# Kernel tuning notes

Hardware: AMD Instinct MI355X
Metric: run time of the kernel (lower is better)

The kernel has to match this reference:

```python
import jax, jax.numpy as jnp
import numpy as np

IN, E, T = 1024, 512, 4096

def _lstm_dir(xs, Wih, Whh, b):
    # xs: [T, E]; Wih: [4E, E]; Whh: [4E, E]; b: [4E] (b_ih + b_hh)
    H = Whh.shape[1]
    def step(carry, xt):
        h, c = carry
        g = xt @ Wih.T + h @ Whh.T + b  # [4E], torch gate order: i, f, g, o
        i, f, gg, o = jnp.split(g, 4)
        i = jax.nn.sigmoid(i); f = jax.nn.sigmoid(f)
        gg = jnp.tanh(gg); o = jax.nn.sigmoid(o)
        c = f * c + i * gg
        h = o * jnp.tanh(c)
        return (h, c), h
    init = (jnp.zeros((H,), xs.dtype), jnp.zeros((H,), xs.dtype))
    _, hs = jax.lax.scan(step, init, xs)
    return hs  # [T, H]

def setup_inputs() -> dict:
    key = jax.random.key(0)
    ks = jax.random.split(key, 12)
    inp = {
        "x": jax.random.normal(ks[0], (1, T, IN), jnp.float32),
        "A": jax.random.normal(ks[1], (IN, E), jnp.float32) * 0.02,
        "B": jax.random.normal(ks[2], (IN, E), jnp.float32) * 0.02,
        "U": jax.random.normal(ks[3], (IN, E), jnp.float32) * 0.02,
        "w_ih_f": jax.random.normal(ks[4], (4 * E, E), jnp.float32) * 0.05,
        "w_hh_f": jax.random.normal(ks[5], (4 * E, E), jnp.float32) * 0.05,
        "b_ih_f": jax.random.normal(ks[6], (4 * E,), jnp.float32) * 0.05,
        "b_hh_f": jnp.zeros((4 * E,), jnp.float32),
        "w_ih_b": jax.random.normal(ks[7], (4 * E, E), jnp.float32) * 0.05,
        "w_hh_b": jax.random.normal(ks[8], (4 * E, E), jnp.float32) * 0.05,
        "b_ih_b": jax.random.normal(ks[9], (4 * E,), jnp.float32) * 0.05,
        "b_hh_b": jnp.zeros((4 * E,), jnp.float32),
        "final_w": jax.random.normal(ks[10], (1, 2 * E), jnp.float32) * 0.05,
        "final_b": jnp.zeros((1,), jnp.float32),
    }
    return inp

def reference(x, A, B, U, w_ih_f, w_hh_f, b_ih_f, b_hh_f,
              w_ih_b, w_hh_b, b_ih_b, b_hh_b, final_w, final_b):
    a = jnp.einsum('bti,ie->bte', x, A)  # [1,T,E]
    b = jnp.einsum('bti,ie->bte', x, B)
    u = jnp.einsum('bti,ie->bte', x, U)
    scores = jnp.einsum('bqe,bke->bqk', u, a)      # unscaled attention [1,T,T]
    p = jax.nn.softmax(scores, axis=-1)
    out_vec = jnp.einsum('bqk,bke->bqe', p, b)     # [1,T,E]
    u_mod = (u * out_vec)[0]                       # gate, batch=1 -> [T,E]
    hf = _lstm_dir(u_mod, w_ih_f, w_hh_f, b_ih_f + b_hh_f)
    hb = _lstm_dir(u_mod[::-1], w_ih_b, w_hh_b, b_ih_b + b_hh_b)[::-1]
    otp = jnp.concatenate([hf, hb], axis=-1)[None]  # [1,T,2E]
    score = jnp.einsum('bte,oe->bto', otp, final_w) + final_b  # [1,T,1]
    return score
```

## Files before the change

### kernel.cpp

```cpp
#include <hip/hip_runtime.h>
#include <cstddef>
#include <cstdint>

#define T_   4096
#define IN_  1024
#define E_   512
#define G4_  2048

typedef unsigned short ushort_t;
typedef __attribute__((ext_vector_type(8))) short bf16x8;
typedef __attribute__((ext_vector_type(4))) float f32x4;

__device__ __forceinline__ ushort_t rne_bf16(float x) {
    unsigned int u = __float_as_uint(x);
    return (ushort_t)((u + 0x7FFFu + ((u >> 16) & 1u)) >> 16);
}
__device__ __forceinline__ float bf2f(ushort_t h) {
    return __uint_as_float((unsigned int)h << 16);
}

__device__ __forceinline__ unsigned long long load_l2_u64(const unsigned long long* p) {
    unsigned long long v;
    asm volatile("global_load_dwordx2 %0, %1, off sc0\n\ts_waitcnt vmcnt(0)"
                 : "=v"(v) : "v"(p) : "memory");
    return v;
}

__global__ __launch_bounds__(256) void mfma_gemm(
    const ushort_t* __restrict__ Ah, const ushort_t* __restrict__ Al,
    const ushort_t* __restrict__ Bh, const ushort_t* __restrict__ Bl,
    float* __restrict__ Cf, ushort_t* __restrict__ Ch, ushort_t* __restrict__ Cl,
    int M, int N, int K, int nA,
    const float* __restrict__ bias1, const float* __restrict__ bias2)
{
    __shared__ ushort_t sAh[128 * 40], sAl[128 * 40];
    __shared__ ushort_t sBh[128 * 40], sBl[128 * 40];

    const int tid  = threadIdx.x;
    const int wv   = tid >> 6;
    const int lane = tid & 63;
    const int quad = lane >> 4;
    const int l16  = lane & 15;
    const int bm = blockIdx.y * 128, bn = blockIdx.x * 128;
    const int wrow = (wv & 1) * 64, wcol = (wv >> 1) * 64;

    f32x4 acc[4][4];
#pragma unroll
    for (int i = 0; i < 4; ++i)
#pragma unroll
        for (int j = 0; j < 4; ++j) acc[i][j] = (f32x4){0.f, 0.f, 0.f, 0.f};

    const int r0 = tid >> 2;
    const int ks = (tid & 3) * 8;

    for (int k0 = 0; k0 < K; k0 += 32) {
        const size_t ga0 = (size_t)(bm + r0) * K + k0 + ks;
        const size_t ga1 = (size_t)(bm + r0 + 64) * K + k0 + ks;
        const size_t gb0 = (size_t)(bn + r0) * K + k0 + ks;
        const size_t gb1 = (size_t)(bn + r0 + 64) * K + k0 + ks;
        uint4 vA0 = *(const uint4*)(Ah + ga0);
        uint4 vA1 = *(const uint4*)(Ah + ga1);
        uint4 vB0h = *(const uint4*)(Bh + gb0);
        uint4 vB1h = *(const uint4*)(Bh + gb1);
        uint4 vB0l = *(const uint4*)(Bl + gb0);
        uint4 vB1l = *(const uint4*)(Bl + gb1);
        uint4 vA0l, vA1l;
        if (nA == 2) { vA0l = *(const uint4*)(Al + ga0); vA1l = *(const uint4*)(Al + ga1); }
        __syncthreads();
        *(uint4*)&sAh[r0 * 40 + ks] = vA0;
        *(uint4*)&sAh[(r0 + 64) * 40 + ks] = vA1;
        *(uint4*)&sBh[r0 * 40 + ks] = vB0h;
        *(uint4*)&sBh[(r0 + 64) * 40 + ks] = vB1h;
        *(uint4*)&sBl[r0 * 40 + ks] = vB0l;
        *(uint4*)&sBl[(r0 + 64) * 40 + ks] = vB1l;
        if (nA == 2) {
            *(uint4*)&sAl[r0 * 40 + ks] = vA0l;
            *(uint4*)&sAl[(r0 + 64) * 40 + ks] = vA1l;
        }
        __syncthreads();

        bf16x8 afh[4], afl[4], bfh[4], bfl[4];
#pragma unroll
        for (int f = 0; f < 4; ++f) {
            const int ar = (wrow + f * 16 + l16) * 40 + quad * 8;
            const int br = (wcol + f * 16 + l16) * 40 + quad * 8;
            afh[f] = *(const bf16x8*)&sAh[ar];
            bfh[f] = *(const bf16x8*)&sBh[br];
            bfl[f] = *(const bf16x8*)&sBl[br];
            if (nA == 2) afl[f] = *(const bf16x8*)&sAl[ar];
        }
#pragma unroll
        for (int fi = 0; fi < 4; ++fi)
#pragma unroll
            for (int fj = 0; fj < 4; ++fj) {
                acc[fi][fj] = __builtin_amdgcn_mfma_f32_16x16x32_bf16(
                    afh[fi], bfh[fj], acc[fi][fj], 0, 0, 0);
                acc[fi][fj] = __builtin_amdgcn_mfma_f32_16x16x32_bf16(
                    afh[fi], bfl[fj], acc[fi][fj], 0, 0, 0);
                if (nA == 2)
                    acc[fi][fj] = __builtin_amdgcn_mfma_f32_16x16x32_bf16(
                        afl[fi], bfh[fj], acc[fi][fj], 0, 0, 0);
            }
    }

#pragma unroll
    for (int fi = 0; fi < 4; ++fi)
#pragma unroll
        for (int fj = 0; fj < 4; ++fj) {
            const int col = bn + wcol + fj * 16 + l16;
            float bv = 0.f;
            if (bias1) bv += bias1[col];
            if (bias2) bv += bias2[col];
#pragma unroll
            for (int r = 0; r < 4; ++r) {
                const int row = bm + wrow + fi * 16 + quad * 4 + r;
                const float v = acc[fi][fj][r] + bv;
                const size_t o = (size_t)row * N + col;
                if (Cf) Cf[o] = v;
                if (Ch) {
                    const ushort_t h = rne_bf16(v);
                    Ch[o] = h;
                    if (Cl) Cl[o] = rne_bf16(v - bf2f(h));
                }
            }
        }
}

__global__ __launch_bounds__(256) void conv_hl(
    const float* __restrict__ in, ushort_t* __restrict__ oh, ushort_t* __restrict__ ol)
{
    const size_t i = ((size_t)blockIdx.x * 256 + threadIdx.x) * 4;
    float4 v = *(const float4*)(in + i);
    ushort4 h, l;
    h.x = rne_bf16(v.x); l.x = rne_bf16(v.x - bf2f(h.x));
    h.y = rne_bf16(v.y); l.y = rne_bf16(v.y - bf2f(h.y));
    h.z = rne_bf16(v.z); l.z = rne_bf16(v.z - bf2f(h.z));
    h.w = rne_bf16(v.w); l.w = rne_bf16(v.w - bf2f(h.w));
    *(ushort4*)(oh + i) = h;
    *(ushort4*)(ol + i) = l;
}

__global__ __launch_bounds__(256) void conv_hl_T(
    const float* __restrict__ in, ushort_t* __restrict__ oh, ushort_t* __restrict__ ol,
    int R, int C)
{
    __shared__ float t[32][33];
    const int tx = threadIdx.x & 31, ty = threadIdx.x >> 5;
    const int gr = blockIdx.y * 32, gc = blockIdx.x * 32;
#pragma unroll
    for (int i = 0; i < 4; ++i)
        t[ty + 8 * i][tx] = in[(size_t)(gr + ty + 8 * i) * C + gc + tx];
    __syncthreads();
#pragma unroll
    for (int i = 0; i < 4; ++i) {
        const int oc = gc + ty + 8 * i;
        const float v = t[tx][ty + 8 * i];
        const ushort_t h = rne_bf16(v);
        oh[(size_t)oc * R + gr + tx] = h;
        ol[(size_t)oc * R + gr + tx] = rne_bf16(v - bf2f(h));
    }
}

__global__ __launch_bounds__(256) void softmax_kernel(
    const float* __restrict__ S, ushort_t* __restrict__ P)
{
    __shared__ float red[8];
    const float* p = S + (size_t)blockIdx.x * T_;
    ushort_t* pr = P + (size_t)blockIdx.x * T_;
    const int tid = threadIdx.x;
    const int wid = tid >> 6;
    const int lane = tid & 63;
    float4 v[4];
#pragma unroll
    for (int i = 0; i < 4; ++i) v[i] = ((const float4*)p)[tid + 256 * i];
    float m = -3.0e38f;
#pragma unroll
    for (int i = 0; i < 4; ++i)
        m = fmaxf(m, fmaxf(fmaxf(v[i].x, v[i].y), fmaxf(v[i].z, v[i].w)));
#pragma unroll
    for (int o = 32; o; o >>= 1) m = fmaxf(m, __shfl_xor(m, o));
    if (lane == 0) red[wid] = m;
    __syncthreads();
    m = fmaxf(fmaxf(red[0], red[1]), fmaxf(red[2], red[3]));
    float s = 0.f;
#pragma unroll
    for (int i = 0; i < 4; ++i) {
        v[i].x = __expf(v[i].x - m); v[i].y = __expf(v[i].y - m);
        v[i].z = __expf(v[i].z - m); v[i].w = __expf(v[i].w - m);
        s += v[i].x + v[i].y + v[i].z + v[i].w;
    }
#pragma unroll
    for (int o = 32; o; o >>= 1) s += __shfl_xor(s, o);
    if (lane == 0) red[4 + wid] = s;
    __syncthreads();
    s = red[4] + red[5] + red[6] + red[7];
    const float inv = 1.f / s;
#pragma unroll
    for (int i = 0; i < 4; ++i) {
        ushort4 o4;
        o4.x = rne_bf16(v[i].x * inv); o4.y = rne_bf16(v[i].y * inv);
        o4.z = rne_bf16(v[i].z * inv); o4.w = rne_bf16(v[i].w * inv);
        ((ushort4*)pr)[tid + 256 * i] = o4;
    }
}

__global__ __launch_bounds__(256) void umod_kernel(
    const ushort_t* __restrict__ uh, const ushort_t* __restrict__ ul,
    const float* __restrict__ ov,
    ushort_t* __restrict__ mh, ushort_t* __restrict__ ml)
{
    const size_t i = ((size_t)blockIdx.x * 256 + threadIdx.x) * 4;
    ushort4 h4 = *(const ushort4*)(uh + i);
    ushort4 l4 = *(const ushort4*)(ul + i);
    float4 o = *(const float4*)(ov + i);
    float4 m;
    m.x = (bf2f(h4.x) + bf2f(l4.x)) * o.x;
    m.y = (bf2f(h4.y) + bf2f(l4.y)) * o.y;
    m.z = (bf2f(h4.z) + bf2f(l4.z)) * o.z;
    m.w = (bf2f(h4.w) + bf2f(l4.w)) * o.w;
    ushort4 oh, ol;
    oh.x = rne_bf16(m.x); ol.x = rne_bf16(m.x - bf2f(oh.x));
    oh.y = rne_bf16(m.y); ol.y = rne_bf16(m.y - bf2f(oh.y));
    oh.z = rne_bf16(m.z); ol.z = rne_bf16(m.z - bf2f(oh.z));
    oh.w = rne_bf16(m.w); ol.w = rne_bf16(m.w - bf2f(oh.w));
    *(ushort4*)(mh + i) = oh;
    *(ushort4*)(ml + i) = ol;
}

#define NU_ 16
#define PACE_L 8L
#define PACE_A 25L

__global__ __launch_bounds__(256, 1) void lstm_kernel(
    const float* __restrict__ whh_f, const float* __restrict__ whh_b,
    const ushort_t* __restrict__ xg_f, const ushort_t* __restrict__ xg_b,
    float* __restrict__ hf_out, float* __restrict__ hb_out,
    unsigned int* __restrict__ hbuf,
    unsigned int* __restrict__ lbuf)
{
    const int xcd = blockIdx.x & 7;
    if (xcd >= 2) return;
    const int dir = xcd;
    const int w   = blockIdx.x >> 3;

    __shared__ float sh[2][4 * 132];

    const int tid  = threadIdx.x;
    const int lane = tid & 63;
    const int j    = tid >> 4;
    const int g    = (tid >> 2) & 3;
    const int c    = tid & 3;
    const int lu   = lane >> 4;
    const int u0   = w * NU_;

    const float* whh = dir ? whh_b : whh_f;
    const ushort_t* xg = dir ? xg_b : xg_f;
    float* hout = dir ? hb_out : hf_out;
    unsigned int* hb = hbuf + dir * 1024;
    unsigned int* lb = lbuf + dir * 1024;

    float wreg[128];
    {
        const float* wr = whh + (size_t)(g * E_ + u0 + j) * E_ + 128 * c;
#pragma unroll
        for (int i = 0; i < 32; ++i)
            *(float4*)&wreg[4 * i] = *(const float4*)(wr + 4 * i);
    }
    for (int i = tid; i < 2 * 4 * 132; i += 256) ((float*)sh)[i] = 0.f;

    float creg = 0.f;
    const float gsc  = (g == 2) ? 2.f : 1.f;
    const float gmul = (g == 2) ? 2.f : 1.f;
    const float gadd = (g == 2) ? -1.f : 0.f;

    float xv = bf2f(xg[(size_t)(dir ? (T_ - 1) : 0) * G4_ + g * E_ + u0 + j]);
    unsigned int budget = 1u << 23;

    const int e0 = 2 * tid;
    const int p0 = (e0 >> 7) * 132 + (e0 & 127);

    long long tpub = (long long)__builtin_amdgcn_s_memrealtime();
    int use_local = 1, failcnt = 0;

    for (int s = 0; s < T_; ++s) {
        const int t = dir ? (T_ - 1 - s) : s;

        if (s > 0) {
            const long long pt = use_local ? PACE_L : PACE_A;
            while ((long long)__builtin_amdgcn_s_memrealtime() - tpub < pt) {}
            const unsigned int tt = (unsigned int)(s - 1) & 0xFFFFu;
            const unsigned long long* srcL =
                (const unsigned long long*)(lb + ((s - 1) & 1) * 512);
            const unsigned long long* srcA =
                (const unsigned long long*)(hb + ((s - 1) & 1) * 512);
            unsigned long long v;
            if (use_local) {
                bool fell = false;
                int spins = 0;
                for (;;) {
                    v = load_l2_u64(srcL + tid);
                    if (((unsigned int)v >> 16) == tt &&
                        ((unsigned int)(v >> 32) >> 16) == tt) break;
                    if (++spins >= 6) {
                        v = __hip_atomic_load(srcA + tid, __ATOMIC_RELAXED,
                                              __HIP_MEMORY_SCOPE_AGENT);
                        if (((unsigned int)v >> 16) == tt &&
                            ((unsigned int)(v >> 32) >> 16) == tt) { fell = true; break; }
                        if (!--budget) break;
                    }
                }
                if (__ballot(fell)) { if (++failcnt >= 8) use_local = 0; }
                else failcnt = 0;
            } else {
                for (;;) {
                    v = __hip_atomic_load(srcA + tid, __ATOMIC_RELAXED,
                                          __HIP_MEMORY_SCOPE_AGENT);
                    if ((((unsigned int)v >> 16) == tt &&
                         ((unsigned int)(v >> 32) >> 16) == tt) || !--budget) break;
                }
            }
            float2 hv;
            hv.x = __uint_as_float((unsigned int)v << 16);
            hv.y = __uint_as_float((unsigned int)(v >> 32) << 16);
            *(float2*)&sh[s & 1][p0] = hv;
        }
        __syncthreads();

        const float* hc = &sh[s & 1][132 * c];
        float sx = 0.f, sy = 0.f, sz = 0.f, sw = 0.f;
#pragma unroll
        for (int i = 0; i < 32; ++i) {
            const float4 h4 = *(const float4*)&hc[4 * i];
            sx = fmaf(wreg[4 * i + 0], h4.x, sx);
            sy = fmaf(wreg[4 * i + 1], h4.y, sy);
            sz = fmaf(wreg[4 * i + 2], h4.z, sz);
            sw = fmaf(wreg[4 * i + 3], h4.w, sw);
        }
        float sum = (sx + sy) + (sz + sw);
        sum += __shfl_xor(sum, 1);
        sum += __shfl_xor(sum, 2);

        const float xx = (sum + xv) * gsc;
        const float rr = __builtin_amdgcn_rcpf(1.f + __expf(-xx));
        const float val = fmaf(rr, gmul, gadd);

        const int base = 16 * lu + c;
        const float iv = __shfl(val, base);
        const float fv = __shfl(val, base + 4);
        const float gv = __shfl(val, base + 8);
        const float ov = __shfl(val, base + 12);
        creg = fmaf(fv, creg, iv * gv);
        const float th = fmaf(2.f, __builtin_amdgcn_rcpf(1.f + __expf(-2.f * creg)), -1.f);
        const float h = ov * th;

        if ((tid & 15) == 0) {
            const unsigned int ub = __float_as_uint(h);
            const unsigned int b16 = (ub + 0x7FFFu + ((ub >> 16) & 1u)) >> 16;
            const unsigned int pkt = (((unsigned int)s & 0xFFFFu) << 16) | b16;
            __hip_atomic_store(lb + (s & 1) * 512 + u0 + j, pkt,
                               __ATOMIC_RELAXED, __HIP_MEMORY_SCOPE_WORKGROUP);
            __hip_atomic_store(hb + (s & 1) * 512 + u0 + j, pkt,
                               __ATOMIC_RELAXED, __HIP_MEMORY_SCOPE_AGENT);
            hout[(size_t)t * E_ + u0 + j] = h;
        }
        tpub = (long long)__builtin_amdgcn_s_memrealtime();

        if (s + 1 < T_)
            xv = bf2f(xg[(size_t)(dir ? (T_ - 2 - s) : (s + 1)) * G4_ + g * E_ + u0 + j]);
    }
}

__global__ __launch_bounds__(256) void final_kernel(
    const float* __restrict__ hf, const float* __restrict__ hb,
    const float* __restrict__ fw, const float* __restrict__ fb,
    float* __restrict__ out)
{
    const int t = blockIdx.x * 4 + (threadIdx.x >> 6);
    const int lane = threadIdx.x & 63;
    float s = 0.f;
#pragma unroll
    for (int i = 0; i < 8; ++i) {
        const int e = lane + 64 * i;
        s += hf[(size_t)t * E_ + e] * fw[e];
    }
#pragma unroll
    for (int i = 0; i < 8; ++i) {
        const int e = lane + 64 * i;
        s += hb[(size_t)t * E_ + e] * fw[E_ + e];
    }
#pragma unroll
    for (int o = 32; o; o >>= 1) s += __shfl_xor(s, o);
    if (lane == 0) out[t] = s + fb[0];
}

extern "C" void kernel_launch(void* const* d_in, const int* in_sizes, int n_in,
                              void* d_out, int out_size, void* d_ws, size_t ws_size,
                              hipStream_t stream)
{
    const float* x     = (const float*)d_in[0];
    const float* Amat  = (const float*)d_in[1];
    const float* Bmat  = (const float*)d_in[2];
    const float* Umat  = (const float*)d_in[3];
    const float* wih_f = (const float*)d_in[4];
    const float* whh_f = (const float*)d_in[5];
    const float* bih_f = (const float*)d_in[6];
    const float* bhh_f = (const float*)d_in[7];
    const float* wih_b = (const float*)d_in[8];
    const float* whh_b = (const float*)d_in[9];
    const float* bih_b = (const float*)d_in[10];
    const float* bhh_b = (const float*)d_in[11];
    const float* fw    = (const float*)d_in[12];
    const float* fb    = (const float*)d_in[13];
    float* out = (float*)d_out;
    char* wsb = (char*)d_ws;
    const size_t MB = 1048576ull;

    ushort_t* uh  = (ushort_t*)(wsb + 0 * MB);
    ushort_t* ul  = (ushort_t*)(wsb + 4 * MB);
    float*    bfp = (float*)   (wsb + 8 * MB);
    ushort_t* xh  = (ushort_t*)(wsb + 16 * MB);
    ushort_t* xl  = (ushort_t*)(wsb + 24 * MB);
    ushort_t* ATh = (ushort_t*)(wsb + 32 * MB);
    ushort_t* ATl = (ushort_t*)(wsb + 33 * MB);
    ushort_t* BTh = (ushort_t*)(wsb + 34 * MB);
    ushort_t* BTl = (ushort_t*)(wsb + 35 * MB);
    ushort_t* UTh = (ushort_t*)(wsb + 36 * MB);
    ushort_t* UTl = (ushort_t*)(wsb + 37 * MB);
    ushort_t* ah  = (ushort_t*)(wsb + 38 * MB);
    ushort_t* al  = (ushort_t*)(wsb + 42 * MB);
    ushort_t* bTh = (ushort_t*)(wsb + 46 * MB);
    ushort_t* bTl = (ushort_t*)(wsb + 50 * MB);
    float*    S_  = (float*)   (wsb + 56 * MB);
    ushort_t* Ph  = (ushort_t*)(wsb + 8 * MB);
    float*    ov_ = (float*)   (wsb + 56 * MB);
    ushort_t* umh = (ushort_t*)(wsb + 64 * MB);
    ushort_t* uml = (ushort_t*)(wsb + 68 * MB);
    ushort_t* wfh = (ushort_t*)(wsb + 72 * MB);
    ushort_t* wfl = (ushort_t*)(wsb + 74 * MB);
    ushort_t* wbh = (ushort_t*)(wsb + 76 * MB);
    ushort_t* wbl = (ushort_t*)(wsb + 78 * MB);
    ushort_t* xfg = (ushort_t*)(wsb + 80 * MB);
    ushort_t* xbg = (ushort_t*)(wsb + 96 * MB);
    float*    hf_ = (float*)   (wsb + 0 * MB);
    float*    hb_ = (float*)   (wsb + 8 * MB);
    unsigned int* hbuf_ = (unsigned int*)(wsb + 112 * MB);
    unsigned int* lbuf_ = (unsigned int*)(wsb + 113 * MB);

    dim3 blk(256);

    conv_hl<<<dim3(4096), blk, 0, stream>>>(x, xh, xl);
    conv_hl_T<<<dim3(16, 32), blk, 0, stream>>>(Amat, ATh, ATl, 1024, 512);
    conv_hl_T<<<dim3(16, 32), blk, 0, stream>>>(Bmat, BTh, BTl, 1024, 512);
    conv_hl_T<<<dim3(16, 32), blk, 0, stream>>>(Umat, UTh, UTl, 1024, 512);
    mfma_gemm<<<dim3(4, 32), blk, 0, stream>>>(xh, xl, ATh, ATl, nullptr, ah, al,
                                               T_, E_, IN_, 2, nullptr, nullptr);
    mfma_gemm<<<dim3(4, 32), blk, 0, stream>>>(xh, xl, BTh, BTl, bfp, nullptr, nullptr,
                                               T_, E_, IN_, 2, nullptr, nullptr);
    mfma_gemm<<<dim3(4, 32), blk, 0, stream>>>(xh, xl, UTh, UTl, nullptr, uh, ul,
                                               T_, E_, IN_, 2, nullptr, nullptr);
    mfma_gemm<<<dim3(32, 32), blk, 0, stream>>>(uh, ul, ah, al, S_, nullptr, nullptr,
                                                T_, T_, E_, 2, nullptr, nullptr);
    conv_hl_T<<<dim3(16, 128), blk, 0, stream>>>(bfp, bTh, bTl, 4096, 512);
    softmax_kernel<<<dim3(T_), blk, 0, stream>>>(S_, Ph);
    mfma_gemm<<<dim3(4, 32), blk, 0, stream>>>(Ph, nullptr, bTh, bTl, ov_, nullptr, nullptr,
                                               T_, E_, T_, 1, nullptr, nullptr);
    umod_kernel<<<dim3(2048), blk, 0, stream>>>(uh, ul, ov_, umh, uml);
    conv_hl<<<dim3(1024), blk, 0, stream>>>(wih_f, wfh, wfl);
    conv_hl<<<dim3(1024), blk, 0, stream>>>(wih_b, wbh, wbl);
    mfma_gemm<<<dim3(16, 32), blk, 0, stream>>>(umh, uml, wfh, wfl, nullptr, xfg, nullptr,
                                                T_, G4_, E_, 2, bih_f, bhh_f);
    mfma_gemm<<<dim3(16, 32), blk, 0, stream>>>(umh, uml, wbh, wbl, nullptr, xbg, nullptr,
                                                T_, G4_, E_, 2, bih_b, bhh_b);
    lstm_kernel<<<dim3(256), blk, 0, stream>>>(whh_f, whh_b, xfg, xbg, hf_, hb_,
                                               hbuf_, lbuf_);
    final_kernel<<<dim3(1024), blk, 0, stream>>>(hf_, hb_, fw, fb, out);
}
```

Before: 6.739 ms.

## Replace per-step block barrier with per-wave h gathering and startup mode consensus

Each wave now loads the whole 512-element previous hidden state into its own LDS slice and polls tags itself, which removes the per-timestep __syncthreads. A one-time probe at kernel start checks whether workgroup-scope L2 stores are visible to all 32 blocks of a direction. The blocks then agree on a single mode, local L2 or agent scope, and store only to that buffer instead of writing both and falling back dynamically. In exchange each wave issues four times as many polling loads per step, uses more LDS, and relies on the startup probe being a correct test of cross-CU visibility.

```diff
diff --git a/kernel.cpp b/kernel.cpp
--- a/kernel.cpp
+++ b/kernel.cpp
@@ -24,6 +24,21 @@
     asm volatile("global_load_dwordx2 %0, %1, off sc0\n\ts_waitcnt vmcnt(0)"
                  : "=v"(v) : "v"(p) : "memory");
     return v;
+}
+__device__ __forceinline__ unsigned int load_l2_u32(const unsigned int* p) {
+    unsigned int v;
+    asm volatile("global_load_dword %0, %1, off sc0\n\ts_waitcnt vmcnt(0)"
+                 : "=v"(v) : "v"(p) : "memory");
+    return v;
+}
+
+__device__ __forceinline__ bool tags8(unsigned long long a, unsigned long long b,
+                                      unsigned long long c, unsigned long long d,
+                                      unsigned int tt) {
+    return ((unsigned int)a >> 16) == tt && (unsigned int)(a >> 48) == tt &&
+           ((unsigned int)b >> 16) == tt && (unsigned int)(b >> 48) == tt &&
+           ((unsigned int)c >> 16) == tt && (unsigned int)(c >> 48) == tt &&
+           ((unsigned int)d >> 16) == tt && (unsigned int)(d >> 48) == tt;
 }
 
 __global__ __launch_bounds__(256) void mfma_gemm(
@@ -236,16 +251,20 @@
     const ushort_t* __restrict__ xg_f, const ushort_t* __restrict__ xg_b,
     float* __restrict__ hf_out, float* __restrict__ hb_out,
     unsigned int* __restrict__ hbuf,
-    unsigned int* __restrict__ lbuf)
+    unsigned int* __restrict__ lbuf,
+    unsigned int* __restrict__ pbuf,
+    unsigned int* __restrict__ vbuf)
 {
     const int xcd = blockIdx.x & 7;
     if (xcd >= 2) return;
     const int dir = xcd;
     const int w   = blockIdx.x >> 3;
 
-    __shared__ float sh[2][4 * 132];
+    __shared__ float sh[4][2][528];
+    __shared__ int smode;
 
     const int tid  = threadIdx.x;
+    const int wv   = tid >> 6;
     const int lane = tid & 63;
     const int j    = tid >> 4;
     const int g    = (tid >> 2) & 3;
@@ -266,7 +285,41 @@
         for (int i = 0; i < 32; ++i)
             *(float4*)&wreg[4 * i] = *(const float4*)(wr + 4 * i);
     }
-    for (int i = tid; i < 2 * 4 * 132; i += 256) ((float*)sh)[i] = 0.f;
+    for (int i = tid; i < 4 * 2 * 528; i += 256) ((float*)sh)[i] = 0.f;
+
+    if (tid == 0)
+        __hip_atomic_store(pbuf + dir * 32 + w, 0x5AFE0001u,
+                           __ATOMIC_RELAXED, __HIP_MEMORY_SCOPE_WORKGROUP);
+    if (tid < 64) {
+        bool seen = true;
+        if (lane < 32) {
+            seen = false;
+            const long long t0 = (long long)__builtin_amdgcn_s_memrealtime();
+            while (!seen) {
+                seen = (load_l2_u32(pbuf + dir * 32 + lane) == 0x5AFE0001u);
+                if (!seen &&
+                    (long long)__builtin_amdgcn_s_memrealtime() - t0 > 1000) break;
+            }
+        }
+        const int allok = (__ballot(seen) == ~0ull) ? 1 : 0;
+        if (lane == 0)
+            __hip_atomic_store(vbuf + dir * 32 + w, 0x7E570000u | (unsigned)allok,
+                               __ATOMIC_RELAXED, __HIP_MEMORY_SCOPE_AGENT);
+        bool vok = true;
+        if (lane < 32) {
+            unsigned int vv = 0, vb = 1u << 22;
+            for (;;) {
+                vv = __hip_atomic_load(vbuf + dir * 32 + lane, __ATOMIC_RELAXED,
+                                       __HIP_MEMORY_SCOPE_AGENT);
+                if ((vv >> 16) == 0x7E57u || !--vb) break;
+            }
+            vok = ((vv >> 16) == 0x7E57u) && (vv & 1u);
+        }
+        const int consensus = (__ballot(vok) == ~0ull) ? 1 : 0;
+        if (lane == 0 && wv == 0) smode = consensus;
+    }
+    __syncthreads();
+    const int mode_local = smode;
 
     float creg = 0.f;
     const float gsc  = (g == 2) ? 2.f : 1.f;
@@ -276,57 +329,57 @@
     float xv = bf2f(xg[(size_t)(dir ? (T_ - 1) : 0) * G4_ + g * E_ + u0 + j]);
     unsigned int budget = 1u << 23;
 
-    const int e0 = 2 * tid;
-    const int p0 = (e0 >> 7) * 132 + (e0 & 127);
-
     long long tpub = (long long)__builtin_amdgcn_s_memrealtime();
-    int use_local = 1, failcnt = 0;
 
     for (int s = 0; s < T_; ++s) {
         const int t = dir ? (T_ - 1 - s) : s;
+        float* shw = sh[wv][s & 1];
 
         if (s > 0) {
-            const long long pt = use_local ? PACE_L : PACE_A;
+            const long long pt = mode_local ? PACE_L : PACE_A;
             while ((long long)__builtin_amdgcn_s_memrealtime() - tpub < pt) {}
             const unsigned int tt = (unsigned int)(s - 1) & 0xFFFFu;
-            const unsigned long long* srcL =
-                (const unsigned long long*)(lb + ((s - 1) & 1) * 512);
-            const unsigned long long* srcA =
-                (const unsigned long long*)(hb + ((s - 1) & 1) * 512);
-            unsigned long long v;
-            if (use_local) {
-                bool fell = false;
-                int spins = 0;
+            const unsigned long long* src = (const unsigned long long*)
+                ((mode_local ? lb : hb) + ((s - 1) & 1) * 512);
+            unsigned long long v0, v1, v2, v3;
+            if (mode_local) {
                 for (;;) {
-                    v = load_l2_u64(srcL + tid);
-                    if (((unsigned int)v >> 16) == tt &&
-                        ((unsigned int)(v >> 32) >> 16) == tt) break;
-                    if (++spins >= 6) {
-                        v = __hip_atomic_load(srcA + tid, __ATOMIC_RELAXED,
-                                              __HIP_MEMORY_SCOPE_AGENT);
-                        if (((unsigned int)v >> 16) == tt &&
-                            ((unsigned int)(v >> 32) >> 16) == tt) { fell = true; break; }
-                        if (!--budget) break;
-                    }
+                    v0 = load_l2_u64(src + lane);
+                    v1 = load_l2_u64(src + lane + 64);
+                    v2 = load_l2_u64(src + lane + 128);
+                    v3 = load_l2_u64(src + lane + 192);
+                    if (tags8(v0, v1, v2, v3, tt) || !--budget) break;
                 }
-                if (__ballot(fell)) { if (++failcnt >= 8) use_local = 0; }
-                else failcnt = 0;
             } else {
                 for (;;) {
-                    v = __hip_atomic_load(srcA + tid, __ATOMIC_RELAXED,
-                                          __HIP_MEMORY_SCOPE_AGENT);
-                    if ((((unsigned int)v >> 16) == tt &&
-                         ((unsigned int)(v >> 32) >> 16) == tt) || !--budget) break;
+                    v0 = __hip_atomic_load(src + lane, __ATOMIC_RELAXED,
+                                           __HIP_MEMORY_SCOPE_AGENT);
+                    v1 = __hip_atomic_load(src + lane + 64, __ATOMIC_RELAXED,
+                                           __HIP_MEMORY_SCOPE_AGENT);
+                    v2 = __hip_atomic_load(src + lane + 128, __ATOMIC_RELAXED,
+                                           __HIP_MEMORY_SCOPE_AGENT);
+                    v3 = __hip_atomic_load(src + lane + 192, __ATOMIC_RELAXED,
+                                           __HIP_MEMORY_SCOPE_AGENT);
+                    if (tags8(v0, v1, v2, v3, tt) || !--budget) break;
                 }
             }
-            float2 hv;
-            hv.x = __uint_as_float((unsigned int)v << 16);
-            hv.y = __uint_as_float((unsigned int)(v >> 32) << 16);
-            *(float2*)&sh[s & 1][p0] = hv;
-        }
-        __syncthreads();
-
-        const float* hc = &sh[s & 1][132 * c];
+            float2 h0, h1, h2, h3;
+            h0.x = __uint_as_float((unsigned int)v0 << 16);
+            h0.y = __uint_as_float((unsigned int)(v0 >> 32) << 16);
+            h1.x = __uint_as_float((unsigned int)v1 << 16);
+            h1.y = __uint_as_float((unsigned int)(v1 >> 32) << 16);
+            h2.x = __uint_as_float((unsigned int)v2 << 16);
+            h2.y = __uint_as_float((unsigned int)(v2 >> 32) << 16);
+            h3.x = __uint_as_float((unsigned int)v3 << 16);
+            h3.y = __uint_as_float((unsigned int)(v3 >> 32) << 16);
+            *(float2*)&shw[2 * lane]           = h0;
+            *(float2*)&shw[132 + 2 * lane]     = h1;
+            *(float2*)&shw[264 + 2 * lane]     = h2;
+            *(float2*)&shw[396 + 2 * lane]     = h3;
+            asm volatile("s_waitcnt lgkmcnt(0)" ::: "memory");
+        }
+
+        const float* hc = &shw[132 * c];
         float sx = 0.f, sy = 0.f, sz = 0.f, sw = 0.f;
 #pragma unroll
         for (int i = 0; i < 32; ++i) {
@@ -357,10 +410,13 @@
             const unsigned int ub = __float_as_uint(h);
             const unsigned int b16 = (ub + 0x7FFFu + ((ub >> 16) & 1u)) >> 16;
             const unsigned int pkt = (((unsigned int)s & 0xFFFFu) << 16) | b16;
-            __hip_atomic_store(lb + (s & 1) * 512 + u0 + j, pkt,
-                               __ATOMIC_RELAXED, __HIP_MEMORY_SCOPE_WORKGROUP);
-            __hip_atomic_store(hb + (s & 1) * 512 + u0 + j, pkt,
-                               __ATOMIC_RELAXED, __HIP_MEMORY_SCOPE_AGENT);
+            if (mode_local) {
+                __hip_atomic_store(lb + (s & 1) * 512 + u0 + j, pkt,
+                                   __ATOMIC_RELAXED, __HIP_MEMORY_SCOPE_WORKGROUP);
+            } else {
+                __hip_atomic_store(hb + (s & 1) * 512 + u0 + j, pkt,
+                                   __ATOMIC_RELAXED, __HIP_MEMORY_SCOPE_AGENT);
+            }
             hout[(size_t)t * E_ + u0 + j] = h;
         }
         tpub = (long long)__builtin_amdgcn_s_memrealtime();
@@ -444,7 +500,9 @@
     float*    hf_ = (float*)   (wsb + 0 * MB);
     float*    hb_ = (float*)   (wsb + 8 * MB);
     unsigned int* hbuf_ = (unsigned int*)(wsb + 112 * MB);
-    unsigned int* lbuf_ = (unsigned int*)(wsb + 113 * MB);
+    unsigned int* lbuf_ = (unsigned int*)(wsb + 112 * MB + 8192);
+    unsigned int* pbuf_ = (unsigned int*)(wsb + 112 * MB + 16384);
+    unsigned int* vbuf_ = (unsigned int*)(wsb + 112 * MB + 20480);
 
     dim3 blk(256);
 
@@ -472,6 +530,6 @@
     mfma_gemm<<<dim3(16, 32), blk, 0, stream>>>(umh, uml, wbh, wbl, nullptr, xbg, nullptr,
                                                 T_, G4_, E_, 2, bih_b, bhh_b);
     lstm_kernel<<<dim3(256), blk, 0, stream>>>(whh_f, whh_b, xfg, xbg, hf_, hb_,
-                                               hbuf_, lbuf_);
+                                               hbuf_, lbuf_, pbuf_, vbuf_);
     final_kernel<<<dim3(1024), blk, 0, stream>>>(hf_, hb_, fw, fb, out);
 }
```

After: 7.124 ms. 5.7% more time.
